# Kernel optimization log

Hardware: AMD Instinct MI355X
Metric: run time of the kernel (lower is better)

## Reference

```python
import jax, jax.numpy as jnp
import numpy as np

KS = 3

def setup_inputs() -> dict:
    key = jax.random.key(0)
    k1, k2, k3 = jax.random.split(key, 3)
    x = jax.random.normal(k1, (4, 4, 256, 36, 36), dtype=jnp.float32)
    target_filter = jax.random.normal(k2, (1024, 256, KS, KS), dtype=jnp.float32) * 0.05
    # per-sample (b=num_img*num_sq=16) positive scale factors; p_n is scaled by ks/offset
    offset = 1.0 + 2.0 * jax.random.uniform(k3, (16, 2), dtype=jnp.float32)
    return {"x": x, "target_filter": target_filter, "offset": offset}


def _deform_sample(xf, offset, ks):
    # xf: [b, ct, h, w] -> bilinearly sampled x_offset: [b, ct, h, w, N], N = ks*ks
    b, ct, h, w = xf.shape
    N = ks * ks
    pad = ks // 2
    xp = jnp.pad(xf, ((0, 0), (0, 0), (pad, pad), (pad, pad)))  # zero padding as in torch
    Hp, Wp = h + 2 * pad, w + 2 * pad
    dt = xf.dtype
    # kernel grid offsets p_n (row-major: n = i*ks + j, i=row/x, j=col/y)
    r = jnp.arange(-(ks - 1) // 2, (ks - 1) // 2 + 1, dtype=dt)
    pnx, pny = jnp.meshgrid(r, r, indexing='ij')
    pnx = pnx.reshape(N)
    pny = pny.reshape(N)
    # base positions p_0 (in padded coordinates)
    p0x = jnp.arange(pad, h + pad, dtype=dt)
    p0y = jnp.arange(pad, w + pad, dtype=dt)
    # per-sample scales ks / offset
    sx = (ks / offset[:, 0])[:, None, None, None]  # [b,1,1,1]
    sy = (ks / offset[:, 1])[:, None, None, None]
    # sampling positions, kept factored: px [b,h,1,N], py [b,1,w,N]
    px = p0x[None, :, None, None] + pnx[None, None, None, :] * sx
    py = p0y[None, None, :, None] + pny[None, None, None, :] * sy
    pxc = jnp.clip(px, 0.0, Hp - 1)
    pyc = jnp.clip(py, 0.0, Wp - 1)
    # integer corners (detached/int in torch as well)
    qltx = jnp.clip(jnp.floor(px), 0.0, Hp - 1)
    qrbx = jnp.clip(jnp.floor(px) + 1.0, 0.0, Hp - 1)
    qlty = jnp.clip(jnp.floor(py), 0.0, Wp - 1)
    qrby = jnp.clip(jnp.floor(py) + 1.0, 0.0, Wp - 1)
    qltx_i = jax.lax.stop_gradient(qltx).astype(jnp.int32)
    qrbx_i = jax.lax.stop_gradient(qrbx).astype(jnp.int32)
    qlty_i = jax.lax.stop_gradient(qlty).astype(jnp.int32)
    qrby_i = jax.lax.stop_gradient(qrby).astype(jnp.int32)
    # bilinear weights, factored per-axis (broadcast b,h,1,N x b,1,w,N)
    gx_l = 1.0 + (jax.lax.stop_gradient(qltx) - pxc)
    gx_r = 1.0 - (jax.lax.stop_gradient(qrbx) - pxc)
    gy_l = 1.0 + (jax.lax.stop_gradient(qlty) - pyc)
    gy_r = 1.0 - (jax.lax.stop_gradient(qrby) - pyc)
    xflat = xp.reshape(b, ct, Hp * Wp)

    def gather(qx, qy):
        idx = jnp.broadcast_to(qx * Wp + qy, (b, h, w, N)).reshape(b, h * w * N)
        g = jax.vmap(lambda xb, ib: jnp.take(xb, ib, axis=1))(xflat, idx)
        return g.reshape(b, ct, h, w, N)

    x_off = ((gx_l * gy_l)[:, None] * gather(qltx_i, qlty_i)
             + (gx_r * gy_r)[:, None] * gather(qrbx_i, qrby_i)
             + (gx_l * gy_r)[:, None] * gather(qltx_i, qrby_i)
             + (gx_r * gy_l)[:, None] * gather(qrbx_i, qlty_i))
    return x_off  # [b, ct, h, w, N]


def reference(x, target_filter, offset):
    # feat_group=False path of DeformConv2d.forward
    ks = target_filter.shape[-1]
    num_img, num_sq, ct, h, w = x.shape
    xf = x.reshape(num_img * num_sq, ct, h, w)
    x_off = _deform_sample(xf, offset, ks)  # [b, ct, h, w, ks*ks]
    out_ch = target_filter.shape[0]
    outg = out_ch // num_sq
    # grouped conv2d with stride=ks over the im2col-style layout == direct einsum
    f = target_filter.reshape(num_sq, outg, ct, ks, ks)
    xo = x_off.reshape(num_img, num_sq, ct, h, w, ks, ks)
    out = jnp.einsum('gocij,mgcyxij->mgoyx', f, xo)
    return out.reshape(num_img, out_ch, h, w)
```

## Files before the change

kernel.cpp:

```cpp
#include <hip/hip_runtime.h>
#include <hip/hip_bf16.h>


#define HH 36
#define WW 36
#define CT 256
#define NB 16
#define KK 2304
#define NP 1296
#define OCH 1024
#define OUTG 256

typedef __attribute__((ext_vector_type(8))) short short8;
typedef __attribute__((ext_vector_type(4))) float f32x4;
typedef __attribute__((ext_vector_type(4))) unsigned short us4;
typedef __attribute__((ext_vector_type(4))) unsigned uint4v;

__device__ __forceinline__ unsigned short f2bf(float v) {
    unsigned u = __float_as_uint(v);
    u += 0x7fffu + ((u >> 16) & 1u);
    return (unsigned short)(u >> 16);
}
__device__ __forceinline__ unsigned pk2bf(float lo, float hi) {
    __hip_bfloat162 h = __float22bfloat162_rn(float2{lo, hi});
    return *reinterpret_cast<unsigned*>(&h);
}

__global__ __launch_bounds__(256) void cvt_filter(const float* __restrict__ f,
                                                  unsigned short* __restrict__ w) {
    const int o = blockIdx.x;
    const float* fo = f + (size_t)o * KK;
    unsigned short* wo = w + (size_t)o * KK;
    for (int k4 = threadIdx.x * 4; k4 < KK; k4 += 1024) {
        int n = k4 >> 8;
        int c = k4 & 255;
        us4 v;
#pragma unroll
        for (int cc = 0; cc < 4; ++cc) v[cc] = f2bf(fo[(c + cc) * 9 + n]);
        *reinterpret_cast<us4*>(wo + k4) = v;
    }
}

__global__ __launch_bounds__(256) void sample_kernel(const float* __restrict__ x,
                                                     const float* __restrict__ off,
                                                     unsigned short* __restrict__ xt) {
    const int wid = (blockIdx.x & 7) * 144 + (blockIdx.x >> 3);
    const int b = wid / 72;
    const int rem = wid - b * 72;
    const int y = rem >> 1;
    const int half = rem & 1;
    const int tid = threadIdx.x;
    const float sx = 3.0f / off[2 * b + 0];
    const float sy = 3.0f / off[2 * b + 1];

    int qxl[3], qxr[3]; float gxl[3], gxr[3];
    bool lok[3], rok[3];
#pragma unroll
    for (int i = 0; i < 3; ++i) {
        float px = (float)(y + 1) + (float)(i - 1) * sx;
        float pc = fminf(fmaxf(px, 0.f), 37.f);
        float fl = floorf(px);
        float ql = fminf(fmaxf(fl, 0.f), 37.f);
        float qr = fminf(fmaxf(fl + 1.f, 0.f), 37.f);
        qxl[i] = (int)ql; qxr[i] = (int)qr;
        gxl[i] = 1.f + (ql - pc);
        gxr[i] = 1.f - (qr - pc);
        lok[i] = (qxl[i] >= 1 && qxl[i] <= 36);
        rok[i] = (qxr[i] >= 1 && qxr[i] <= 36);
    }

    __shared__ int   s_qyl[HH * 3], s_qyr[HH * 3];
    __shared__ float s_gyl[HH * 3], s_gyr[HH * 3];
    if (tid < HH * 3) {
        int xx = tid / 3, j = tid % 3;
        float py = (float)(xx + 1) + (float)(j - 1) * sy;
        float pc = fminf(fmaxf(py, 0.f), 37.f);
        float fl = floorf(py);
        float ql = fminf(fmaxf(fl, 0.f), 37.f);
        float qr = fminf(fmaxf(fl + 1.f, 0.f), 37.f);
        s_qyl[tid] = (int)ql; s_qyr[tid] = (int)qr;
        s_gyl[tid] = 1.f + (ql - pc);
        s_gyr[tid] = 1.f - (qr - pc);
    }

    __shared__ float xr[3 * 38 * 64];

    for (int chunk = 0; chunk < 2; ++chunk) {
        const int c0 = half * 128 + chunk * 64;
        __syncthreads();

        for (int t = tid; t < 384; t += 256) {
            int i = t / 128, r3 = t & 127;
            int col = (r3 & 64) ? 37 : 0, c = r3 & 63;
            xr[(i * 38 + col) * 64 + c] = 0.f;
        }

        const float* xb = x + (size_t)(b * CT + c0) * NP;
        for (int t = tid; t < 3 * 64 * 9; t += 256) {
            const int i = t / 576;
            const int r2 = t - i * 576;
            const int c = r2 / 9;
            const int cq = r2 - c * 9;
            const int colb = 1 + cq * 4;
            const float* xc = xb + c * NP;
            float4 vl = make_float4(0.f, 0.f, 0.f, 0.f);
            float4 vr = vl;
            if (lok[i]) vl = *(const float4*)(xc + (qxl[i] - 1) * WW + colb - 1);
            if (rok[i]) vr = *(const float4*)(xc + (qxr[i] - 1) * WW + colb - 1);
            float* dst = &xr[(i * 38 + colb) * 64 + c];
            dst[0]   = gxl[i] * vl.x + gxr[i] * vr.x;
            dst[64]  = gxl[i] * vl.y + gxr[i] * vr.y;
            dst[128] = gxl[i] * vl.z + gxr[i] * vr.z;
            dst[192] = gxl[i] * vl.w + gxr[i] * vr.w;
        }
        __syncthreads();

        for (int t = tid; t < 3 * 36 * 8; t += 256) {
            const int i = t / 288;
            const int r = t - i * 288;
            const int xi = r >> 3;
            const int c8 = r & 7;
            unsigned short* op = xt + ((size_t)b * NP + y * WW + xi) * KK + c0 + c8 * 8
                               + i * 3 * 256;
#pragma unroll
            for (int j = 0; j < 3; ++j) {
                const int tq = xi * 3 + j;
                const float gl = s_gyl[tq], gr = s_gyr[tq];
                const float* L = &xr[(i * 38 + s_qyl[tq]) * 64 + c8 * 8];
                const float* R = &xr[(i * 38 + s_qyr[tq]) * 64 + c8 * 8];
                f32x4 L0 = *(const f32x4*)L, L1 = *(const f32x4*)(L + 4);
                f32x4 R0 = *(const f32x4*)R, R1 = *(const f32x4*)(R + 4);
                uint4v w;
                w[0] = pk2bf(gl * L0[0] + gr * R0[0], gl * L0[1] + gr * R0[1]);
                w[1] = pk2bf(gl * L0[2] + gr * R0[2], gl * L0[3] + gr * R0[3]);
                w[2] = pk2bf(gl * L1[0] + gr * R1[0], gl * L1[1] + gr * R1[1]);
                w[3] = pk2bf(gl * L1[2] + gr * R1[2], gl * L1[3] + gr * R1[3]);
                *reinterpret_cast<uint4v*>(op + j * 256) = w;
            }
        }
    }
}

__global__ __launch_bounds__(256) void gemm_kernel(const unsigned short* __restrict__ wbf,
                                                   const unsigned short* __restrict__ xt,
                                                   float* __restrict__ out) {
    const int wid = (blockIdx.x & 7) * 84 + (blockIdx.x >> 3);
    const int b = wid / 42;
    const int rem = wid - b * 42;
    const int mt = rem / 21;
    const int nt = rem - mt * 21;
    const int m0 = mt * 128;
    const int p0 = nt * 64;
    const int g = b & 3;
    const int mimg = b >> 2;

    const unsigned short* Ab = wbf + (size_t)(g * OUTG + m0) * KK;
    const unsigned short* Bb = xt + (size_t)b * NP * KK;

    __shared__ __align__(16) unsigned short As[2][128 * 64];
    __shared__ __align__(16) unsigned short Bs[2][64 * 64];

    const int tid = threadIdx.x;
    const int wave = tid >> 6, lane = tid & 63;
    const int wr = wave >> 1, wc = wave & 1;
    const int l8 = lane >> 3;
    const int sgrp = (lane & 7) ^ l8;

    f32x4 acc[4][2] = {};

#define STAGE(BUF, KT) do {                                                       \
    const int k0_ = (KT) * 64;                                                    \
    _Pragma("unroll")                                                             \
    for (int ii = 0; ii < 4; ++ii) {                                              \
        const int inst = wave * 4 + ii;                                           \
        const int row = inst * 8 + l8;                                            \
        const unsigned short* srcA = Ab + (size_t)row * KK + k0_ + sgrp * 8;      \
        __builtin_amdgcn_global_load_lds(                                         \
            (const __attribute__((address_space(1))) void*)srcA,                  \
            (__attribute__((address_space(3))) void*)&As[BUF][inst * 512], 16, 0, 0); \
    }                                                                             \
    _Pragma("unroll")                                                             \
    for (int ii = 0; ii < 2; ++ii) {                                              \
        const int inst = wave * 2 + ii;                                           \
        const int row = inst * 8 + l8;                                            \
        int prow = p0 + row;                                                      \
        prow = prow < NP ? prow : NP - 1;                                         \
        const unsigned short* srcB = Bb + (size_t)prow * KK + k0_ + sgrp * 8;     \
        __builtin_amdgcn_global_load_lds(                                         \
            (const __attribute__((address_space(1))) void*)srcB,                  \
            (__attribute__((address_space(3))) void*)&Bs[BUF][inst * 512], 16, 0, 0); \
    }                                                                             \
} while (0)

#define COMPUTE(BUF) do {                                                         \
    _Pragma("unroll")                                                             \
    for (int kk = 0; kk < 2; ++kk) {                                              \
        short8 a[4], bfr[2];                                                      \
        const int g8 = (((kk * 4) + (lane >> 4)) ^ (lane & 7)) << 3;              \
        const int rA = wr * 64 + (lane & 15);                                     \
        const int rB = wc * 32 + (lane & 15);                                     \
        _Pragma("unroll")                                                         \
        for (int m = 0; m < 4; ++m)                                               \
            a[m] = *(const short8*)&As[BUF][(rA + m * 16) * 64 + g8];             \
        _Pragma("unroll")                                                         \
        for (int n = 0; n < 2; ++n)                                               \
            bfr[n] = *(const short8*)&Bs[BUF][(rB + n * 16) * 64 + g8];           \
        _Pragma("unroll")                                                         \
        for (int m = 0; m < 4; ++m)                                               \
            _Pragma("unroll")                                                     \
            for (int n = 0; n < 2; ++n)                                           \
                acc[m][n] = __builtin_amdgcn_mfma_f32_16x16x32_bf16(              \
                    a[m], bfr[n], acc[m][n], 0, 0, 0);                            \
    }                                                                             \
} while (0)

    STAGE(0, 0);

#pragma unroll 1
    for (int kt = 0; kt < 35; ++kt) {
        STAGE((kt + 1) & 1, kt + 1);
        asm volatile("s_waitcnt vmcnt(6)" ::: "memory");
        __builtin_amdgcn_sched_barrier(0);
        __builtin_amdgcn_s_barrier();
        COMPUTE(kt & 1);
        __builtin_amdgcn_s_barrier();
    }
    asm volatile("s_waitcnt vmcnt(0)" ::: "memory");
    __builtin_amdgcn_sched_barrier(0);
    __builtin_amdgcn_s_barrier();
    COMPUTE(35 & 1);

#undef STAGE
#undef COMPUTE

    float* ob = out + ((size_t)mimg * OCH + g * OUTG) * NP;
    const int o0 = m0 + wr * 64 + ((lane >> 4) << 2);
    const int pc = p0 + wc * 32 + (lane & 15);
#pragma unroll
    for (int n = 0; n < 2; ++n) {
        int p = pc + n * 16;
        if (p >= NP) continue;
#pragma unroll
        for (int m = 0; m < 4; ++m) {
#pragma unroll
            for (int r = 0; r < 4; ++r)
                ob[(size_t)(o0 + m * 16 + r) * NP + p] = acc[m][n][r];
        }
    }
}

extern "C" void kernel_launch(void* const* d_in, const int* in_sizes, int n_in,
                              void* d_out, int out_size, void* d_ws, size_t ws_size,
                              hipStream_t stream) {
    const float* x   = (const float*)d_in[0];
    const float* tf  = (const float*)d_in[1];
    const float* off = (const float*)d_in[2];
    float* out = (float*)d_out;

    unsigned short* xt  = (unsigned short*)d_ws;
    unsigned short* wbf = xt + (size_t)NB * NP * KK;

    hipLaunchKernelGGL(cvt_filter, dim3(OCH), dim3(256), 0, stream, tf, wbf);
    hipLaunchKernelGGL(sample_kernel, dim3(NB * HH * 2), dim3(256), 0, stream, x, off, xt);
    hipLaunchKernelGGL(gemm_kernel, dim3(672), dim3(256), 0, stream, wbf, xt, out);
}
```

Measured before the change: 71.39 us.

## Fuse filter conversion into sample kernel and XOR-swizzle LDS row buffer

Filter bf16 conversion is merged into the sampling kernel as extra blocks, removing one kernel launch and letting both jobs run concurrently. The row buffer in LDS now uses an XOR swizzle of the channel group by column to reduce bank conflicts on the strided scalar writes and vector reads. The swizzle adds index arithmetic, and the merged grid mixes two kinds of work that may finish unevenly.

```diff
diff --git a/kernel.cpp b/kernel.cpp
--- a/kernel.cpp
+++ b/kernel.cpp
@@ -10,6 +10,7 @@
 #define NP 1296
 #define OCH 1024
 #define OUTG 256
+#define SAMPLE_BLOCKS (NB * HH * 2)
 
 typedef __attribute__((ext_vector_type(8))) short short8;
 typedef __attribute__((ext_vector_type(4))) float f32x4;
@@ -26,25 +27,28 @@
     return *reinterpret_cast<unsigned*>(&h);
 }
 
-__global__ __launch_bounds__(256) void cvt_filter(const float* __restrict__ f,
-                                                  unsigned short* __restrict__ w) {
-    const int o = blockIdx.x;
-    const float* fo = f + (size_t)o * KK;
-    unsigned short* wo = w + (size_t)o * KK;
-    for (int k4 = threadIdx.x * 4; k4 < KK; k4 += 1024) {
-        int n = k4 >> 8;
-        int c = k4 & 255;
-        us4 v;
-#pragma unroll
-        for (int cc = 0; cc < 4; ++cc) v[cc] = f2bf(fo[(c + cc) * 9 + n]);
-        *reinterpret_cast<us4*>(wo + k4) = v;
-    }
-}
-
 __global__ __launch_bounds__(256) void sample_kernel(const float* __restrict__ x,
+                                                     const float* __restrict__ tf,
                                                      const float* __restrict__ off,
-                                                     unsigned short* __restrict__ xt) {
-    const int wid = (blockIdx.x & 7) * 144 + (blockIdx.x >> 3);
+                                                     unsigned short* __restrict__ xt,
+                                                     unsigned short* __restrict__ wbf) {
+    const int bx = blockIdx.x;
+    if (bx >= SAMPLE_BLOCKS) {
+        const int o = bx - SAMPLE_BLOCKS;
+        const float* fo = tf + (size_t)o * KK;
+        unsigned short* wo = wbf + (size_t)o * KK;
+        for (int k4 = threadIdx.x * 4; k4 < KK; k4 += 1024) {
+            int n = k4 >> 8;
+            int c = k4 & 255;
+            us4 v;
+#pragma unroll
+            for (int cc = 0; cc < 4; ++cc) v[cc] = f2bf(fo[(c + cc) * 9 + n]);
+            *reinterpret_cast<us4*>(wo + k4) = v;
+        }
+        return;
+    }
+
+    const int wid = (bx & 7) * 144 + (bx >> 3);
     const int b = wid / 72;
     const int rem = wid - b * 72;
     const int y = rem >> 1;
@@ -107,11 +111,14 @@
             float4 vr = vl;
             if (lok[i]) vl = *(const float4*)(xc + (qxl[i] - 1) * WW + colb - 1);
             if (rok[i]) vr = *(const float4*)(xc + (qxr[i] - 1) * WW + colb - 1);
-            float* dst = &xr[(i * 38 + colb) * 64 + c];
-            dst[0]   = gxl[i] * vl.x + gxr[i] * vr.x;
-            dst[64]  = gxl[i] * vl.y + gxr[i] * vr.y;
-            dst[128] = gxl[i] * vl.z + gxr[i] * vr.z;
-            dst[192] = gxl[i] * vl.w + gxr[i] * vr.w;
+            float v[4] = { gxl[i] * vl.x + gxr[i] * vr.x, gxl[i] * vl.y + gxr[i] * vr.y,
+                           gxl[i] * vl.z + gxr[i] * vr.z, gxl[i] * vl.w + gxr[i] * vr.w };
+            const int ch = c >> 3, co = c & 7;
+#pragma unroll
+            for (int k = 0; k < 4; ++k) {
+                const int col = colb + k;
+                xr[(i * 38 + col) * 64 + ((ch ^ (col & 7)) << 3) + co] = v[k];
+            }
         }
         __syncthreads();
 
@@ -125,9 +132,10 @@
 #pragma unroll
             for (int j = 0; j < 3; ++j) {
                 const int tq = xi * 3 + j;
+                const int ql = s_qyl[tq], qr = s_qyr[tq];
                 const float gl = s_gyl[tq], gr = s_gyr[tq];
-                const float* L = &xr[(i * 38 + s_qyl[tq]) * 64 + c8 * 8];
-                const float* R = &xr[(i * 38 + s_qyr[tq]) * 64 + c8 * 8];
+                const float* L = &xr[(i * 38 + ql) * 64 + ((c8 ^ (ql & 7)) << 3)];
+                const float* R = &xr[(i * 38 + qr) * 64 + ((c8 ^ (qr & 7)) << 3)];
                 f32x4 L0 = *(const f32x4*)L, L1 = *(const f32x4*)(L + 4);
                 f32x4 R0 = *(const f32x4*)R, R1 = *(const f32x4*)(R + 4);
                 uint4v w;
@@ -260,7 +268,7 @@
     unsigned short* xt  = (unsigned short*)d_ws;
     unsigned short* wbf = xt + (size_t)NB * NP * KK;
 
-    hipLaunchKernelGGL(cvt_filter, dim3(OCH), dim3(256), 0, stream, tf, wbf);
-    hipLaunchKernelGGL(sample_kernel, dim3(NB * HH * 2), dim3(256), 0, stream, x, off, xt);
+    hipLaunchKernelGGL(sample_kernel, dim3(SAMPLE_BLOCKS + OCH), dim3(256), 0, stream,
+                       x, tf, off, xt, wbf);
     hipLaunchKernelGGL(gemm_kernel, dim3(672), dim3(256), 0, stream, wbf, xt, out);
 }
```

Result: faster. 67.17 us (median of 2 runs) (-5.9%).
